# Kernel tuning notes

Hardware: AMD Instinct MI355X
Metric: run time of the kernel (lower is better)

The kernel has to match this reference:

```python
import jax, jax.numpy as jnp
from jax import lax
import numpy as np

EPS = 1e-12      # F.normalize eps
TOP_N = 250      # top negatives selected
SMOOTH = 1e-5    # soft dice smooth


def _dilate10(m):
    # == 10 iterations of 3x3x3 binary max-pool dilation. m: [B,D,H,W] float.
    for _ in range(10):
        m = lax.reduce_window(m, 0.0, lax.max, (1, 3, 3, 3), (1, 1, 1, 1), 'SAME')
    return m


def _self_loss(feature, lab):
    # feature: [B,C,D,H,W], lab: [B,D,H,W] int
    feat = jnp.moveaxis(feature, 1, -1)                       # [B,D,H,W,C]
    pos = (lab == 1)
    posf = pos.astype(feat.dtype)
    cnt = posf.sum()
    std = (feat * posf[..., None]).sum((0, 1, 2, 3)) / jnp.maximum(cnt, 1.0)
    std = jnp.where(cnt > 0, std, 0.0)                        # [C]
    std_n = std / jnp.maximum(jnp.linalg.norm(std), EPS)
    feat_n = feat / jnp.maximum(jnp.linalg.norm(feat, axis=-1, keepdims=True), EPS)
    # cosine similarity of per-voxel normalized features vs normalized mean positive
    sim = jnp.einsum('bdhwc,c->bdhw', feat_n, std_n)

    # positive term: mean over positives of (1 - sim)
    pos_loss = jnp.where(cnt > 0, ((1.0 - sim) * posf).sum() / jnp.maximum(cnt, 1.0), 0.0)

    # easily-misclassified ring: dilate(pos,10) & ~pos; mean relu(sim)
    mis = (_dilate10(posf) > 0) & (~pos)
    misf = mis.astype(sim.dtype)
    mcnt = misf.sum()
    mis_loss = jnp.where(mcnt > 0, (jax.nn.relu(sim) * misf).sum() / jnp.maximum(mcnt, 1.0), 0.0)

    # hard negatives: top-250 sims among label==0, scatter to mask, dilate, & ~pos
    neg = (lab == 0)
    neg_sims = jnp.where(neg, sim, -jnp.inf).reshape(-1)
    top_vals, top_idx = lax.top_k(neg_sims, TOP_N)
    hsm = jnp.zeros(neg_sims.shape[0], sim.dtype).at[top_idx].set(
        jnp.where(jnp.isfinite(top_vals), 1.0, 0.0)).reshape(sim.shape)
    fin = (_dilate10(hsm) > 0) & (~pos)
    finf = fin.astype(sim.dtype)
    fcnt = finf.sum()
    neg_loss = jnp.where(fcnt > 0, (jax.nn.relu(sim) * finf).sum() / jnp.maximum(fcnt, 1.0), 0.0)

    return pos_loss + mis_loss + neg_loss


def _ce_dice(net_output, target):
    lab = target[:, 0]                                        # [B,D,H,W]
    logp = jax.nn.log_softmax(net_output, axis=1)
    ce = -jnp.mean(jnp.take_along_axis(logp, target, axis=1))
    probs = jnp.exp(logp)                                     # softmax_helper_dim1
    nc = net_output.shape[1]
    onehot = jax.nn.one_hot(lab, nc, axis=1, dtype=probs.dtype)  # [B,nc,D,H,W]
    axes = (0, 2, 3, 4)                                       # batch_dice=True
    tp = (probs * onehot).sum(axes)
    fp = (probs * (1.0 - onehot)).sum(axes)
    fn = ((1.0 - probs) * onehot).sum(axes)
    dc = (2.0 * tp + SMOOTH) / (2.0 * tp + fp + fn + SMOOTH + 1e-8)
    dice = -jnp.mean(dc[1:])                                  # do_bg=False
    return ce, dice


def reference(feature, net_output, target):
    ce, dice = _ce_dice(net_output, target)
    sl = _self_loss(feature, target[:, 0])
    return 1.0 * ce + 1.0 * dice + 5.0 * sl


def setup_inputs():
    key = jax.random.key(0)
    k1, k2, k3 = jax.random.split(key, 3)
    B, C, D, H, W = 2, 32, 64, 128, 128
    NC = 2
    feature = jax.random.normal(k1, (B, C, D, H, W), jnp.float32)
    net_output = jax.random.normal(k2, (B, NC, D, H, W), jnp.float32)
    target = jax.random.randint(k3, (B, 1, D, H, W), 0, 2).astype(jnp.int32)
    return {'feature': feature, 'net_output': net_output, 'target': target}
```

## Files before the change

kernel.cpp:

```cpp
#include <hip/hip_runtime.h>
#include <stdint.h>

typedef unsigned int u32;
typedef unsigned long long u64;

#define BB 2
#define CC 32
#define DD 64
#define HH 128
#define WW 128
#define SS (DD*HH*WW)
#define NN (BB*SS)
#define NQ (NN/4)
#define NWORDS (NN/64)
#define EPSF 1e-12f
#define TOPN 250u

struct Ctrl {
  u32 done4, tie, pad0, pad1;
};

struct Acc {
  double ce, tp, fp, fn;
  double stdsum[CC];
  double pos_num, mis_num, fin_num;
  u64 cnt, mcnt, fcnt;
};

__device__ __forceinline__ float waveRedF(float v){
#pragma unroll
  for (int o = 32; o; o >>= 1) v += __shfl_xor(v, o);
  return v;
}
__device__ __forceinline__ u32 waveRedU(u32 v){
#pragma unroll
  for (int o = 32; o; o >>= 1) v += __shfl_xor(v, o);
  return v;
}
__device__ __forceinline__ void red_d(double* dst, float v, volatile float* sh){
  int lane = threadIdx.x & 63, wid = threadIdx.x >> 6;
  v = waveRedF(v);
  if (lane == 0) sh[wid] = v;
  __syncthreads();
  if (threadIdx.x == 0){
    float t = 0.f;
    for (int i = 0; i < (int)(blockDim.x >> 6); i++) t += sh[i];
    atomicAdd(dst, (double)t);
  }
  __syncthreads();
}
__device__ __forceinline__ void red_u(u64* dst, u32 v, volatile u32* sh){
  int lane = threadIdx.x & 63, wid = threadIdx.x >> 6;
  v = waveRedU(v);
  if (lane == 0) sh[wid] = v;
  __syncthreads();
  if (threadIdx.x == 0){
    u32 t = 0;
    for (int i = 0; i < (int)(blockDim.x >> 6); i++) t += sh[i];
    atomicAdd(dst, (u64)t);
  }
  __syncthreads();
}

__device__ __forceinline__ u32 sortkey(float f){
  u32 u = __float_as_uint(f);
  return (u & 0x80000000u) ? ~u : (u | 0x80000000u);
}

__device__ __forceinline__ void select_top(const u32* __restrict__ hist, u32 nbins,
                                           u32 k, u32* shres, u32* binOut, u32* kremOut){
  __syncthreads();
  if (threadIdx.x < 64){
    int lane = threadIdx.x;
    u32 running = 0; bool found = false;
    for (u32 chunk = 0; chunk * 64 < nbins && !found; chunk++){
      int bin = (int)nbins - 1 - (int)(chunk * 64 + (u32)lane);
      u32 val = (bin >= 0) ? hist[bin] : 0u;
      u32 p = val;
#pragma unroll
      for (int o = 1; o < 64; o <<= 1){ u32 t = __shfl_up(p, o); if (lane >= o) p += t; }
      u32 tot = __shfl(p, 63);
      u32 incl = running + p, excl = incl - val;
      bool hit = (excl < k) && (incl >= k);
      u64 mb = __ballot(hit);
      if (mb){
        int hl = __ffsll((unsigned long long)mb) - 1;
        if (lane == hl){ shres[0] = (u32)bin; shres[1] = k - excl; }
        found = true;
      } else running += tot;
    }
    if (!found && lane == 0){ shres[0] = 0; shres[1] = k; }
  }
  __syncthreads();
  *binOut = shres[0]; *kremOut = shres[1];
}

__global__ __launch_bounds__(256) void k_main1(const float* __restrict__ feat,
                                               const float* __restrict__ net,
                                               const int* __restrict__ tgt,
                                               u64* __restrict__ pbits, Acc* acc){
  __shared__ u32 nibsh[256];
  __shared__ float sacc[CC];
  __shared__ float shf[4]; __shared__ u32 shu[4];
  float a[CC];
#pragma unroll
  for (int c = 0; c < CC; c++) a[c] = 0.f;
  float ce = 0.f, tp = 0.f, fp = 0.f, fnn = 0.f;
  u32 cnt = 0;
  const u32 stride = 1024u * 256u;
#pragma unroll 1
  for (u32 it = 0; it < 2; it++){
    u32 q = blockIdx.x * 256u + threadIdx.x + it * stride;
    u32 v = q * 4u;
    u32 b = v >> 20, s = v & (SS - 1);
    int4 l4 = *(const int4*)(tgt + v);
    u32 nib = (l4.x ? 1u : 0u) | (l4.y ? 2u : 0u) | (l4.z ? 4u : 0u) | (l4.w ? 8u : 0u);
    cnt += __popc(nib);
    __syncthreads();
    nibsh[threadIdx.x] = nib;
    {
      const float* nb = net + (size_t)(b * 2) * SS + s;
      float4 x0 = *(const float4*)(nb);
      float4 x1 = *(const float4*)(nb + SS);
      float xs0[4] = {x0.x, x0.y, x0.z, x0.w};
      float xs1[4] = {x1.x, x1.y, x1.z, x1.w};
#pragma unroll
      for (int j = 0; j < 4; j++){
        int lab = (nib >> j) & 1;
        float m = fmaxf(xs0[j], xs1[j]);
        float lse = m + logf(expf(xs0[j] - m) + expf(xs1[j] - m));
        ce += lse - (lab ? xs1[j] : xs0[j]);
        float p1 = expf(xs1[j] - lse);
        if (lab){ tp += p1; fnn += 1.0f - p1; } else fp += p1;
      }
    }
    {
      float4 p;
      p.x = (nib & 1) ? 1.f : 0.f; p.y = (nib & 2) ? 1.f : 0.f;
      p.z = (nib & 4) ? 1.f : 0.f; p.w = (nib & 8) ? 1.f : 0.f;
      const float* fb = feat + (size_t)b * CC * SS + s;
#pragma unroll 1
      for (int c0 = 0; c0 < CC; c0 += 8){
#pragma unroll
        for (int c = 0; c < 8; c++){
          float4 f = *(const float4*)(fb + (size_t)(c0 + c) * SS);
          a[c0 + c] += f.x * p.x + f.y * p.y + f.z * p.z + f.w * p.w;
        }
      }
    }
    __syncthreads();
    if (threadIdx.x < 16){
      u64 o = 0;
#pragma unroll
      for (int j = 0; j < 16; j++)
        o |= (u64)(nibsh[threadIdx.x * 16 + j] & 0xFu) << (4 * j);
      pbits[blockIdx.x * 16u + it * 16384u + threadIdx.x] = o;
    }
  }
  for (u32 i = threadIdx.x; i < CC; i += 256u) sacc[i] = 0.f;
  __syncthreads();
  int lane = threadIdx.x & 63;
#pragma unroll 1
  for (int c = 0; c < CC; c++){
    float vv = waveRedF(a[c]);
    if (lane == 0) atomicAdd(&sacc[c], vv);
  }
  __syncthreads();
  if (threadIdx.x < CC) atomicAdd(&acc->stdsum[threadIdx.x], (double)sacc[threadIdx.x]);
  red_d(&acc->ce, ce, shf);
  red_d(&acc->tp, tp, shf);
  red_d(&acc->fp, fp, shf);
  red_d(&acc->fn, fnn, shf);
  red_u(&acc->cnt, cnt, shu);
}

__global__ __launch_bounds__(256) void k_sim(const float* __restrict__ feat,
                                             const u64* __restrict__ pbits,
                                             Acc* acc, float* __restrict__ sim,
                                             u32* __restrict__ h1){
  __shared__ float st[CC];
  __shared__ u32 lh[2048];
  __shared__ float shf[4];
  {
    u64 cnt = acc->cnt;
    float sv = 0.f;
    if (threadIdx.x < CC && cnt) sv = (float)(acc->stdsum[threadIdx.x] / (double)cnt);
    if (threadIdx.x < 64){
      float t = waveRedF(sv * sv);
      float d = fmaxf(sqrtf(t), EPSF);
      if (threadIdx.x < CC) st[threadIdx.x] = sv / d;
    }
  }
  for (u32 i = threadIdx.x; i < 2048u; i += 256u) lh[i] = 0;
  __syncthreads();
  float pn = 0.f;
  const u32 stride = 1024u * 256u;
#pragma unroll 1
  for (u32 it = 0; it < 2; it++){
    u32 q = blockIdx.x * 256u + threadIdx.x + it * stride;
    u32 v = q * 4u;
    u32 b = v >> 20, s = v & (SS - 1);
    u32 nib = (u32)(pbits[q >> 4] >> ((q & 15u) << 2)) & 0xFu;
    const float* fb = feat + (size_t)b * CC * SS + s;
    float4 dot = {0,0,0,0}, n2 = {0,0,0,0};
#pragma unroll 1
    for (int c0 = 0; c0 < CC; c0 += 8){
#pragma unroll
      for (int c = 0; c < 8; c++){
        float4 f = *(const float4*)(fb + (size_t)(c0 + c) * SS);
        float w = st[c0 + c];
        dot.x += f.x * w; dot.y += f.y * w; dot.z += f.z * w; dot.w += f.w * w;
        n2.x += f.x * f.x; n2.y += f.y * f.y; n2.z += f.z * f.z; n2.w += f.w * f.w;
      }
    }
    float4 sm;
    sm.x = dot.x / fmaxf(sqrtf(n2.x), EPSF);
    sm.y = dot.y / fmaxf(sqrtf(n2.y), EPSF);
    sm.z = dot.z / fmaxf(sqrtf(n2.z), EPSF);
    sm.w = dot.w / fmaxf(sqrtf(n2.w), EPSF);
    *(float4*)(sim + v) = sm;
    float ss[4] = {sm.x, sm.y, sm.z, sm.w};
#pragma unroll
    for (int j = 0; j < 4; j++){
      if ((nib >> j) & 1u) pn += 1.f - ss[j];
      else atomicAdd(&lh[sortkey(ss[j]) >> 21], 1u);
    }
  }
  __syncthreads();
  for (u32 i = threadIdx.x; i < 2048u; i += 256u)
    if (lh[i]) atomicAdd(&h1[i], lh[i]);
  red_d(&acc->pos_num, pn, shf);
}

__device__ __forceinline__ void dilwh_slab(const u64* __restrict__ in, u64* __restrict__ out,
                                           u32 slab, u64* arr){
  u32 base = slab * 256u;
  int t = threadIdx.x;
  if (t < 128){
    u64 lo = in[base + 2 * t], hi = in[base + 2 * t + 1];
    u64 al = lo, ah = hi;
#pragma unroll
    for (int i = 0; i < 10; i++){ u64 c = al >> 63; ah = ah | (ah << 1) | c; al = al | (al << 1); }
    u64 bl = lo, bh = hi;
#pragma unroll
    for (int i = 0; i < 10; i++){ u64 c = bh << 63; bl = bl | (bl >> 1) | c; bh = bh | (bh >> 1); }
    arr[2 * t] = al | bl;
    arr[2 * t + 1] = ah | bh;
  }
  __syncthreads();
  int h = t >> 1, wj = t & 1;
  int h0 = h - 10 > 0 ? h - 10 : 0;
  int h1 = h + 10 < 127 ? h + 10 : 127;
  u64 o = 0;
  for (int hh = h0; hh <= h1; hh++) o |= arr[2 * hh + wj];
  out[base + (u32)t] = o;
  __syncthreads();
}

__global__ __launch_bounds__(256) void k_dilwh(const u64* __restrict__ in, u64* __restrict__ out){
  __shared__ u64 arr[256];
  dilwh_slab(in, out, blockIdx.x, arr);
}

__global__ __launch_bounds__(256) void k_histL2(const float* __restrict__ sim,
                                                const u64* __restrict__ pbits,
                                                const u32* __restrict__ h1,
                                                u32* __restrict__ h2,
                                                const u64* __restrict__ P,
                                                u64* __restrict__ T1P){
  __shared__ u64 arr[256];
  __shared__ u32 lh[2048];
  __shared__ u32 shres[2];
  if (blockIdx.x < 128u) dilwh_slab(P, T1P, blockIdx.x, arr);
  u32 p1, k1;
  select_top(h1, 2048, TOPN, shres, &p1, &k1);
  for (u32 i = threadIdx.x; i < 2048u; i += 256u) lh[i] = 0;
  __syncthreads();
  const u32 stride = 512u * 256u;
#pragma unroll 1
  for (u32 it = 0; it < 4; it++){
    u32 q = blockIdx.x * 256u + threadIdx.x + it * stride;
    u32 nib = (u32)(pbits[q >> 4] >> ((q & 15u) << 2)) & 0xFu;
    float4 s4 = *(const float4*)(sim + q * 4u);
    float ss[4] = {s4.x, s4.y, s4.z, s4.w};
#pragma unroll
    for (int j = 0; j < 4; j++){
      if (!((nib >> j) & 1u)){
        u32 key = sortkey(ss[j]);
        if ((key >> 21) == p1) atomicAdd(&lh[(key >> 10) & 2047u], 1u);
      }
    }
  }
  __syncthreads();
  for (u32 i = threadIdx.x; i < 2048u; i += 256u)
    if (lh[i]) atomicAdd(&h2[i], lh[i]);
}

__global__ __launch_bounds__(256) void k_mark(const float* __restrict__ sim,
                                              const u64* __restrict__ pbits,
                                              u64* __restrict__ hs,
                                              const u32* __restrict__ h1,
                                              const u32* __restrict__ h2,
                                              Ctrl* ctrl){
  __shared__ u32 shres[2];
  u32 p1, k1, b2, k2;
  select_top(h1, 2048, TOPN, shres, &p1, &k1);
  select_top(h2, 2048, k1, shres, &b2, &k2);
  u32 p12 = (p1 << 11) | b2;
  int lane = threadIdx.x & 63;
  const u32 stride = 1024u * 256u;
#pragma unroll 1
  for (u32 it = 0; it < 8; it++){
    u32 v = blockIdx.x * 256u + threadIdx.x + it * stride;
    u64 w = pbits[v >> 6];
    bool neg = !((w >> (v & 63u)) & 1ull);
    bool seed = false;
    if (neg){
      u32 pref = sortkey(sim[v]) >> 10;
      if (pref > p12) seed = true;
      else if (pref == p12){
        u32 old = atomicAdd(&ctrl->tie, 1u);
        if (old < k2) seed = true;
      }
    }
    u64 mb = __ballot(seed);
    if (lane == 0) hs[v >> 6] = mb;
  }
}

__global__ __launch_bounds__(256) void k_final(const float* __restrict__ sim,
                                               const u64* __restrict__ P,
                                               const u64* __restrict__ T1P,
                                               const u64* __restrict__ T1H,
                                               Acc* acc, Ctrl* ctrl, float* out){
  __shared__ float shf[4]; __shared__ u32 shu[4];
  __shared__ int amLast;
  u32 wi = blockIdx.x * 256u + threadIdx.x;
  u32 wj = wi & 1u;
  u32 row = wi >> 1;
  int h = (int)(row & 127u);
  int d = (int)((row >> 7) & 63u);
  u32 b = row >> 13;
  int d0 = d - 10 > 0 ? d - 10 : 0;
  int d1 = d + 10 < 63 ? d + 10 : 63;
  const u64* bp = T1P + ((size_t)(b << 13) + (u32)h) * 2 + wj;
  const u64* bh = T1H + ((size_t)(b << 13) + (u32)h) * 2 + wj;
  u64 dpw = 0, dhw = 0;
  for (int dd = d0; dd <= d1; dd++){
    dpw |= bp[(size_t)dd * 256];
    dhw |= bh[(size_t)dd * 256];
  }
  u64 pw = P[wi];
  u64 mis = dpw & ~pw;
  u64 fin = dhw & ~pw;
  float mn = 0.f, fnm = 0.f;
  u32 mc = (u32)__popcll(mis), fc = (u32)__popcll(fin);
  const float* sp = sim + (size_t)wi * 64u;
#pragma unroll 1
  for (int jj = 0; jj < 16; jj++){
    float4 s4 = *(const float4*)(sp + jj * 4);
    float ss[4] = {s4.x, s4.y, s4.z, s4.w};
#pragma unroll
    for (int j = 0; j < 4; j++){
      int bit = jj * 4 + j;
      float r = fmaxf(ss[j], 0.f);
      if ((mis >> bit) & 1ull) mn += r;
      if ((fin >> bit) & 1ull) fnm += r;
    }
  }
  red_d(&acc->mis_num, mn, shf);
  red_d(&acc->fin_num, fnm, shf);
  red_u(&acc->mcnt, mc, shu);
  red_u(&acc->fcnt, fc, shu);
  __threadfence();
  if (threadIdx.x == 0) amLast = (atomicAdd(&ctrl->done4, 1u) == gridDim.x - 1);
  __syncthreads();
  if (amLast && threadIdx.x == 0){
    double ce = acc->ce / (double)NN;
    double tp = acc->tp, fp = acc->fp, fn = acc->fn;
    double dc1 = (2.0 * tp + 1e-5) / (2.0 * tp + fp + fn + 1e-5 + 1e-8);
    u64 cnt = acc->cnt;
    double pos_loss = cnt ? (acc->pos_num / (double)cnt) : 0.0;
    u64 mcnt = atomicAdd(&acc->mcnt, 0ull);
    u64 fcnt = atomicAdd(&acc->fcnt, 0ull);
    double mis_loss = mcnt ? (atomicAdd(&acc->mis_num, 0.0) / (double)mcnt) : 0.0;
    double neg_loss = fcnt ? (atomicAdd(&acc->fin_num, 0.0) / (double)fcnt) : 0.0;
    out[0] = (float)(ce - dc1 + 5.0 * (pos_loss + mis_loss + neg_loss));
  }
}

extern "C" void kernel_launch(void* const* d_in, const int* in_sizes, int n_in,
                              void* d_out, int out_size, void* d_ws, size_t ws_size,
                              hipStream_t stream){
  (void)in_sizes; (void)n_in; (void)out_size; (void)ws_size;
  const float* feat = (const float*)d_in[0];
  const float* net  = (const float*)d_in[1];
  const int*   tgt  = (const int*)d_in[2];
  float* out = (float*)d_out;
  char* ws = (char*)d_ws;

  size_t off = 0;
  auto take = [&](size_t bytes) -> void* {
    void* p = (void*)(ws + off);
    off += (bytes + 255) & ~(size_t)255;
    return p;
  };
  float* sim = (float*)take((size_t)NN * 4);
  u64* P   = (u64*)take((size_t)NWORDS * 8);
  u64* T1P = (u64*)take((size_t)NWORDS * 8);
  u64* HS  = (u64*)take((size_t)NWORDS * 8);
  u64* T1H = (u64*)take((size_t)NWORDS * 8);
  size_t zstart = off;
  u32* h1 = (u32*)take(2048 * 4);
  u32* h2 = (u32*)take(2048 * 4);
  Ctrl* ctrl = (Ctrl*)take(sizeof(Ctrl));
  Acc* acc = (Acc*)take(sizeof(Acc));
  hipMemsetAsync(ws + zstart, 0, off - zstart, stream);

  k_main1<<<1024, 256, 0, stream>>>(feat, net, tgt, P, acc);
  k_sim<<<1024, 256, 0, stream>>>(feat, P, acc, sim, h1);
  k_histL2<<<512, 256, 0, stream>>>(sim, P, h1, h2, P, T1P);
  k_mark<<<1024, 256, 0, stream>>>(sim, P, HS, h1, h2, ctrl);
  k_dilwh<<<128, 256, 0, stream>>>(HS, T1H);
  k_final<<<128, 256, 0, stream>>>(sim, P, T1P, T1H, acc, ctrl, out);
}
```

Baseline: 538.9 us.

## Split positive-mean feature sum into per-channel kernel and retile similarity pass

Moves the per-channel masked feature sum out of the CE kernel into a new kernel where each block handles one channel over a 64K-voxel chunk. This removes the 32-register accumulator array and the serial 32-channel wave reductions per block. The similarity kernel now processes four float4 groups per thread over contiguous voxels with half the blocks, giving more independent loads in flight per channel. It adds one kernel launch, and the feature tensor is still read in both the std and sim passes.

```diff
diff --git a/kernel.cpp b/kernel.cpp
--- a/kernel.cpp
+++ b/kernel.cpp
@@ -95,16 +95,11 @@
   *binOut = shres[0]; *kremOut = shres[1];
 }
 
-__global__ __launch_bounds__(256) void k_main1(const float* __restrict__ feat,
-                                               const float* __restrict__ net,
-                                               const int* __restrict__ tgt,
-                                               u64* __restrict__ pbits, Acc* acc){
+__global__ __launch_bounds__(256) void k_ce(const float* __restrict__ net,
+                                            const int* __restrict__ tgt,
+                                            u64* __restrict__ pbits, Acc* acc){
   __shared__ u32 nibsh[256];
-  __shared__ float sacc[CC];
   __shared__ float shf[4]; __shared__ u32 shu[4];
-  float a[CC];
-#pragma unroll
-  for (int c = 0; c < CC; c++) a[c] = 0.f;
   float ce = 0.f, tp = 0.f, fp = 0.f, fnn = 0.f;
   u32 cnt = 0;
   const u32 stride = 1024u * 256u;
@@ -134,20 +129,6 @@
         if (lab){ tp += p1; fnn += 1.0f - p1; } else fp += p1;
       }
     }
-    {
-      float4 p;
-      p.x = (nib & 1) ? 1.f : 0.f; p.y = (nib & 2) ? 1.f : 0.f;
-      p.z = (nib & 4) ? 1.f : 0.f; p.w = (nib & 8) ? 1.f : 0.f;
-      const float* fb = feat + (size_t)b * CC * SS + s;
-#pragma unroll 1
-      for (int c0 = 0; c0 < CC; c0 += 8){
-#pragma unroll
-        for (int c = 0; c < 8; c++){
-          float4 f = *(const float4*)(fb + (size_t)(c0 + c) * SS);
-          a[c0 + c] += f.x * p.x + f.y * p.y + f.z * p.z + f.w * p.w;
-        }
-      }
-    }
     __syncthreads();
     if (threadIdx.x < 16){
       u64 o = 0;
@@ -157,21 +138,40 @@
       pbits[blockIdx.x * 16u + it * 16384u + threadIdx.x] = o;
     }
   }
-  for (u32 i = threadIdx.x; i < CC; i += 256u) sacc[i] = 0.f;
-  __syncthreads();
-  int lane = threadIdx.x & 63;
-#pragma unroll 1
-  for (int c = 0; c < CC; c++){
-    float vv = waveRedF(a[c]);
-    if (lane == 0) atomicAdd(&sacc[c], vv);
-  }
-  __syncthreads();
-  if (threadIdx.x < CC) atomicAdd(&acc->stdsum[threadIdx.x], (double)sacc[threadIdx.x]);
   red_d(&acc->ce, ce, shf);
   red_d(&acc->tp, tp, shf);
   red_d(&acc->fp, fp, shf);
   red_d(&acc->fn, fnn, shf);
   red_u(&acc->cnt, cnt, shu);
+}
+
+__global__ __launch_bounds__(256) void k_std(const float* __restrict__ feat,
+                                             const u64* __restrict__ pbits, Acc* acc){
+  u32 c = blockIdx.x & 31u;
+  u32 chunk = blockIdx.x >> 5;
+  u32 vbase = chunk * 65536u;
+  u32 b = vbase >> 20;
+  u32 s0 = vbase & (SS - 1);
+  const float* fp = feat + (size_t)b * CC * SS + (size_t)c * SS + s0;
+  const u64* pb = pbits + (vbase >> 6);
+  float a = 0.f;
+#pragma unroll 8
+  for (u32 i = 0; i < 64; i++){
+    u32 off = i * 1024u + threadIdx.x * 4u;
+    float4 f = *(const float4*)(fp + off);
+    u32 bits = (u32)(pb[off >> 6] >> (off & 63u)) & 0xFu;
+    if (bits & 1u) a += f.x;
+    if (bits & 2u) a += f.y;
+    if (bits & 4u) a += f.z;
+    if (bits & 8u) a += f.w;
+  }
+  __shared__ float sh[4];
+  int lane = threadIdx.x & 63, wid = threadIdx.x >> 6;
+  a = waveRedF(a);
+  if (lane == 0) sh[wid] = a;
+  __syncthreads();
+  if (threadIdx.x == 0)
+    atomicAdd(&acc->stdsum[c], (double)(sh[0] + sh[1] + sh[2] + sh[3]));
 }
 
 __global__ __launch_bounds__(256) void k_sim(const float* __restrict__ feat,
@@ -193,36 +193,48 @@
   }
   for (u32 i = threadIdx.x; i < 2048u; i += 256u) lh[i] = 0;
   __syncthreads();
+  u32 vbase = blockIdx.x * 4096u;
+  u32 b = vbase >> 20;
+  u32 s0 = vbase & (SS - 1);
+  const float* fp = feat + (size_t)b * CC * SS + s0;
+  float4 dt[4], n2[4];
+#pragma unroll
+  for (int g = 0; g < 4; g++){
+    dt[g].x = dt[g].y = dt[g].z = dt[g].w = 0.f;
+    n2[g].x = n2[g].y = n2[g].z = n2[g].w = 0.f;
+  }
+#pragma unroll 2
+  for (u32 c = 0; c < CC; c++){
+    float w = st[c];
+    const float* fc = fp + (size_t)c * SS;
+    float4 f[4];
+#pragma unroll
+    for (int g = 0; g < 4; g++)
+      f[g] = *(const float4*)(fc + (u32)g * 1024u + threadIdx.x * 4u);
+#pragma unroll
+    for (int g = 0; g < 4; g++){
+      dt[g].x += f[g].x * w; dt[g].y += f[g].y * w;
+      dt[g].z += f[g].z * w; dt[g].w += f[g].w * w;
+      n2[g].x += f[g].x * f[g].x; n2[g].y += f[g].y * f[g].y;
+      n2[g].z += f[g].z * f[g].z; n2[g].w += f[g].w * f[g].w;
+    }
+  }
   float pn = 0.f;
-  const u32 stride = 1024u * 256u;
-#pragma unroll 1
-  for (u32 it = 0; it < 2; it++){
-    u32 q = blockIdx.x * 256u + threadIdx.x + it * stride;
-    u32 v = q * 4u;
-    u32 b = v >> 20, s = v & (SS - 1);
-    u32 nib = (u32)(pbits[q >> 4] >> ((q & 15u) << 2)) & 0xFu;
-    const float* fb = feat + (size_t)b * CC * SS + s;
-    float4 dot = {0,0,0,0}, n2 = {0,0,0,0};
-#pragma unroll 1
-    for (int c0 = 0; c0 < CC; c0 += 8){
-#pragma unroll
-      for (int c = 0; c < 8; c++){
-        float4 f = *(const float4*)(fb + (size_t)(c0 + c) * SS);
-        float w = st[c0 + c];
-        dot.x += f.x * w; dot.y += f.y * w; dot.z += f.z * w; dot.w += f.w * w;
-        n2.x += f.x * f.x; n2.y += f.y * f.y; n2.z += f.z * f.z; n2.w += f.w * f.w;
-      }
-    }
+#pragma unroll
+  for (int g = 0; g < 4; g++){
+    u32 off = (u32)g * 1024u + threadIdx.x * 4u;
+    u32 v = vbase + off;
     float4 sm;
-    sm.x = dot.x / fmaxf(sqrtf(n2.x), EPSF);
-    sm.y = dot.y / fmaxf(sqrtf(n2.y), EPSF);
-    sm.z = dot.z / fmaxf(sqrtf(n2.z), EPSF);
-    sm.w = dot.w / fmaxf(sqrtf(n2.w), EPSF);
+    sm.x = dt[g].x / fmaxf(sqrtf(n2[g].x), EPSF);
+    sm.y = dt[g].y / fmaxf(sqrtf(n2[g].y), EPSF);
+    sm.z = dt[g].z / fmaxf(sqrtf(n2[g].z), EPSF);
+    sm.w = dt[g].w / fmaxf(sqrtf(n2[g].w), EPSF);
     *(float4*)(sim + v) = sm;
+    u32 bits = (u32)(pbits[v >> 6] >> (v & 63u)) & 0xFu;
     float ss[4] = {sm.x, sm.y, sm.z, sm.w};
 #pragma unroll
     for (int j = 0; j < 4; j++){
-      if ((nib >> j) & 1u) pn += 1.f - ss[j];
+      if ((bits >> j) & 1u) pn += 1.f - ss[j];
       else atomicAdd(&lh[sortkey(ss[j]) >> 21], 1u);
     }
   }
@@ -417,8 +429,9 @@
   Acc* acc = (Acc*)take(sizeof(Acc));
   hipMemsetAsync(ws + zstart, 0, off - zstart, stream);
 
-  k_main1<<<1024, 256, 0, stream>>>(feat, net, tgt, P, acc);
-  k_sim<<<1024, 256, 0, stream>>>(feat, P, acc, sim, h1);
+  k_ce<<<1024, 256, 0, stream>>>(net, tgt, P, acc);
+  k_std<<<1024, 256, 0, stream>>>(feat, P, acc);
+  k_sim<<<512, 256, 0, stream>>>(feat, P, acc, sim, h1);
   k_histL2<<<512, 256, 0, stream>>>(sim, P, h1, h2, P, T1P);
   k_mark<<<1024, 256, 0, stream>>>(sim, P, HS, h1, h2, ctrl);
   k_dilwh<<<128, 256, 0, stream>>>(HS, T1H);
```

New measurement: 533.7 us. Within noise of the previous version (-1.0%).
